# Kernel tuning notes

Hardware: AMD Instinct MI355X
Metric: run time of the kernel (lower is better)

The kernel has to match this reference:

```python
import jax, jax.numpy as jnp
import numpy as np

N_ENT = 100000
D = 128
N_EDGES = 1600000
B = 8192
EPS = 1e-5


def setup_inputs() -> dict:
    key = jax.random.key(0)
    ks = jax.random.split(key, 12)
    return {
        "E": jax.random.normal(ks[0], (N_ENT, D), jnp.float32),
        "gamma": jnp.ones((D,), jnp.float32),
        "beta": jnp.zeros((D,), jnp.float32),
        "W_gnn": jax.random.normal(ks[1], (D, D), jnp.float32) / np.sqrt(D),
        "b_gnn": jnp.zeros((D,), jnp.float32),
        "W_g": jax.random.normal(ks[2], (D,), jnp.float32) / np.sqrt(D),
        "b_g": jnp.zeros((), jnp.float32),
        "W_age": jax.random.normal(ks[3], (D, 7), jnp.float32) / np.sqrt(D),
        "b_age": jnp.zeros((7,), jnp.float32),
        "W_occ": jax.random.normal(ks[4], (D, 21), jnp.float32) / np.sqrt(D),
        "b_occ": jnp.zeros((21,), jnp.float32),
        "src": jax.random.randint(ks[5], (N_EDGES,), 0, N_ENT, jnp.int32),
        "dst": jax.random.randint(ks[6], (N_EDGES,), 0, N_ENT, jnp.int32),
        "neighbor": jax.random.randint(ks[7], (B,), 0, N_ENT, jnp.int32),
        "gender": jax.random.randint(ks[8], (B,), 0, 2, jnp.int32),
        "age": jax.random.randint(ks[9], (B,), 0, 7, jnp.int32),
        "occupation": jax.random.randint(ks[10], (B,), 0, 21, jnp.int32),
    }


def reference(E, gamma, beta, W_gnn, b_gnn, W_g, b_g, W_age, b_age, W_occ, b_occ,
              src, dst, neighbor, gender, age, occupation):
    n = E.shape[0]
    # encoder (embedding of all nodes) -> batchnorm over node axis
    mu = jnp.mean(E, axis=0)
    var = jnp.var(E, axis=0)
    h = (E - mu) * jax.lax.rsqrt(var + EPS) * gamma + beta  # [N, D]
    # gnn: mean neighbor aggregation over edge list, then linear + relu
    agg = jax.ops.segment_sum(h[src], dst, num_segments=n)  # [N, D]
    deg = jax.ops.segment_sum(jnp.ones_like(src, jnp.float32), dst, num_segments=n)
    agg = agg / jnp.maximum(deg, 1.0)[:, None]
    h = jax.nn.relu(agg @ W_gnn + b_gnn)  # [N, D]
    # gather walked-to nodes; gradient-reversal layer is identity in forward
    u = h[neighbor]  # [B, D]
    gender_pred = u @ W_g + b_g            # [B]
    age_pred = u @ W_age + b_age           # [B, 7]
    occ_pred = u @ W_occ + b_occ           # [B, 21]
    # mode == 'gender': BCEWithLogitsLoss (mean)
    z = gender.astype(jnp.float32)
    x = gender_pred
    loss_adv = jnp.mean(jnp.maximum(x, 0.0) - x * z + jnp.log1p(jnp.exp(-jnp.abs(x))))
    return (loss_adv, age_pred, gender_pred, occ_pred)
```

## Files before the change

### kernel.cpp

```cpp
#include <hip/hip_runtime.h>
#include <hip/hip_bf16.h>
#include <math.h>

#define N_ENT   100000
#define DIM     128
#define N_EDGES 1600000
#define BATCH   8192
#define EPS     1e-5f
#define CAP     64
#define NSTAT_BLK   512
#define NGATHER_BLK (BATCH / 4)

#define WS_SCALE     256
#define WS_SHIFT     384
#define WS_COUNT     512
#define WS_BCOUNT    528
#define WS_SLOTOF    8720
#define WS_BUCKET    108720
#define WS_SLOTHEAD  633008
#define WS_PARTIAL   895152
#define WS_HSUM      1026224

__global__ __launch_bounds__(256) void init_mark_kernel(const int* __restrict__ neighbor,
                                                        int* __restrict__ slot_of,
                                                        int* __restrict__ bcount,
                                                        int* __restrict__ count,
                                                        float* __restrict__ out_loss) {
    int n = blockIdx.x * 256 + threadIdx.x;
    if (n < BATCH) {
        bcount[n] = 0;
        slot_of[neighbor[n]] = -2;
    }
    if (n < 16) count[n] = 0;
    if (n == 0) out_loss[0] = 0.f;
}

__global__ __launch_bounds__(256) void compact_kernel(int* __restrict__ slot_of,
                                                      int* __restrict__ count) {
    int n = blockIdx.x * 256 + threadIdx.x;
    bool marked = (n < N_ENT && slot_of[n] == -2);
    unsigned long long m = __ballot(marked);
    int lane = threadIdx.x & 63;
    int wid = threadIdx.x >> 6;
    int prefix = __popcll(m & ((1ull << lane) - 1ull));
    __shared__ int wsum[4];
    __shared__ int base;
    if (lane == 0) wsum[wid] = __popcll(m);
    __syncthreads();
    if (threadIdx.x == 0) {
        base = atomicAdd(count, wsum[0] + wsum[1] + wsum[2] + wsum[3]);
    }
    __syncthreads();
    int wbase = 0;
    for (int i = 0; i < wid; ++i) wbase += wsum[i];
    if (marked) slot_of[n] = base + wbase + prefix;
}

__global__ __launch_bounds__(256) void edge_bucket_kernel(const int4* __restrict__ src4,
                                                          const int4* __restrict__ dst4,
                                                          const int* __restrict__ slot_of,
                                                          int* __restrict__ bcount,
                                                          int* __restrict__ bucket) {
    const int n4 = N_EDGES / 4;
    int tid = blockIdx.x * blockDim.x + threadIdx.x;
    int e0 = tid * 2;
    int e1 = tid * 2 + 1;
    if (e0 >= n4) return;
    int4 d0 = dst4[e0];
    int4 s0 = src4[e0];
    bool has1 = (e1 < n4);
    int4 d1 = has1 ? dst4[e1] : make_int4(0, 0, 0, 0);
    int4 s1 = has1 ? src4[e1] : make_int4(0, 0, 0, 0);
    int sl0 = slot_of[d0.x];
    int sl1 = slot_of[d0.y];
    int sl2 = slot_of[d0.z];
    int sl3 = slot_of[d0.w];
    int sl4 = has1 ? slot_of[d1.x] : -1;
    int sl5 = has1 ? slot_of[d1.y] : -1;
    int sl6 = has1 ? slot_of[d1.z] : -1;
    int sl7 = has1 ? slot_of[d1.w] : -1;
    if (sl0 >= 0) { int p = atomicAdd(&bcount[sl0], 1); if (p < CAP) bucket[sl0 * CAP + p] = s0.x; }
    if (sl1 >= 0) { int p = atomicAdd(&bcount[sl1], 1); if (p < CAP) bucket[sl1 * CAP + p] = s0.y; }
    if (sl2 >= 0) { int p = atomicAdd(&bcount[sl2], 1); if (p < CAP) bucket[sl2 * CAP + p] = s0.z; }
    if (sl3 >= 0) { int p = atomicAdd(&bcount[sl3], 1); if (p < CAP) bucket[sl3 * CAP + p] = s0.w; }
    if (sl4 >= 0) { int p = atomicAdd(&bcount[sl4], 1); if (p < CAP) bucket[sl4 * CAP + p] = s1.x; }
    if (sl5 >= 0) { int p = atomicAdd(&bcount[sl5], 1); if (p < CAP) bucket[sl5 * CAP + p] = s1.y; }
    if (sl6 >= 0) { int p = atomicAdd(&bcount[sl6], 1); if (p < CAP) bucket[sl6 * CAP + p] = s1.z; }
    if (sl7 >= 0) { int p = atomicAdd(&bcount[sl7], 1); if (p < CAP) bucket[sl7 * CAP + p] = s1.w; }
}

__global__ __launch_bounds__(256) void stats_gather_kernel(const float4* __restrict__ E4,
                                                           const int* __restrict__ count,
                                                           const int* __restrict__ bcount,
                                                           const int* __restrict__ bucket,
                                                           float* __restrict__ hsum,
                                                           float* __restrict__ partial) {
    int t = threadIdx.x;
    if (blockIdx.x < NGATHER_BLK) {
        int slot = blockIdx.x * 4 + (t >> 6);
        int U = count[0];
        if (slot >= U) return;
        int lane = t & 63;
        int q = lane & 31;
        int sub = lane >> 5;
        int dg = bcount[slot];
        int m = dg < CAP ? dg : CAP;
        const int* bk = bucket + slot * CAP;
        float ax = 0.f, ay = 0.f, az = 0.f, aw = 0.f;
        int i = sub;
        for (; i + 6 < m; i += 8) {
            int r0 = bk[i], r1 = bk[i + 2], r2 = bk[i + 4], r3 = bk[i + 6];
            float4 v0 = E4[(size_t)r0 * 32 + q];
            float4 v1 = E4[(size_t)r1 * 32 + q];
            float4 v2 = E4[(size_t)r2 * 32 + q];
            float4 v3 = E4[(size_t)r3 * 32 + q];
            ax += v0.x + v1.x + v2.x + v3.x;
            ay += v0.y + v1.y + v2.y + v3.y;
            az += v0.z + v1.z + v2.z + v3.z;
            aw += v0.w + v1.w + v2.w + v3.w;
        }
        for (; i < m; i += 2) {
            int r0 = bk[i];
            float4 v0 = E4[(size_t)r0 * 32 + q];
            ax += v0.x; ay += v0.y; az += v0.z; aw += v0.w;
        }
        ax += __shfl_down(ax, 32);
        ay += __shfl_down(ay, 32);
        az += __shfl_down(az, 32);
        aw += __shfl_down(aw, 32);
        if (sub == 0) {
            float4 o; o.x = ax; o.y = ay; o.z = az; o.w = aw;
            ((float4*)(hsum + (size_t)slot * DIM))[q] = o;
        }
        return;
    }
    int sid = blockIdx.x - NGATHER_BLK;
    int cg = t & 31;
    int rs = t >> 5;
    const int STRIDE = NSTAT_BLK * 8;
    float sx = 0.f, sy = 0.f, sz = 0.f, sw = 0.f;
    float qx = 0.f, qy = 0.f, qz = 0.f, qw = 0.f;
    const float4 z4 = make_float4(0.f, 0.f, 0.f, 0.f);
    for (int r = sid * 8 + rs; r < N_ENT; r += 4 * STRIDE) {
        int r1 = r + STRIDE, r2 = r + 2 * STRIDE, r3 = r + 3 * STRIDE;
        float4 v0 = E4[(size_t)r * 32 + cg];
        float4 v1 = (r1 < N_ENT) ? E4[(size_t)r1 * 32 + cg] : z4;
        float4 v2 = (r2 < N_ENT) ? E4[(size_t)r2 * 32 + cg] : z4;
        float4 v3 = (r3 < N_ENT) ? E4[(size_t)r3 * 32 + cg] : z4;
        sx += v0.x + v1.x + v2.x + v3.x;
        sy += v0.y + v1.y + v2.y + v3.y;
        sz += v0.z + v1.z + v2.z + v3.z;
        sw += v0.w + v1.w + v2.w + v3.w;
        qx += v0.x * v0.x + v1.x * v1.x + v2.x * v2.x + v3.x * v3.x;
        qy += v0.y * v0.y + v1.y * v1.y + v2.y * v2.y + v3.y * v3.y;
        qz += v0.z * v0.z + v1.z * v1.z + v2.z * v2.z + v3.z * v3.z;
        qw += v0.w * v0.w + v1.w * v1.w + v2.w * v2.w + v3.w * v3.w;
    }
    __shared__ float sh[8 * 256];
    sh[0 * 256 + t] = sx; sh[1 * 256 + t] = sy;
    sh[2 * 256 + t] = sz; sh[3 * 256 + t] = sw;
    sh[4 * 256 + t] = qx; sh[5 * 256 + t] = qy;
    sh[6 * 256 + t] = qz; sh[7 * 256 + t] = qw;
    __syncthreads();
    for (int o = 128; o >= 32; o >>= 1) {
        if (t < o) {
#pragma unroll
            for (int j = 0; j < 8; ++j) sh[j * 256 + t] += sh[j * 256 + t + o];
        }
        __syncthreads();
    }
    if (t < 32) {
#pragma unroll
        for (int j = 0; j < 8; ++j)
            partial[sid * 256 + j * 32 + t] = sh[j * 256 + t];
    }
}

__global__ __launch_bounds__(256) void finalize_kernel(const float* __restrict__ partial,
                                                       const float* __restrict__ gamma,
                                                       const float* __restrict__ beta,
                                                       float* __restrict__ scale,
                                                       float* __restrict__ shift) {
    int t = threadIdx.x;
    float s = 0.f;
    for (int b = 0; b < NSTAT_BLK; ++b) s += partial[b * 256 + t];
    __shared__ float tot[256];
    tot[t] = s;
    __syncthreads();
    if (t < 128) {
        int ti = t >> 2, j = t & 3;
        const float invn = 1.0f / (float)N_ENT;
        float mu = tot[j * 32 + ti] * invn;
        float var = tot[(j + 4) * 32 + ti] * invn - mu * mu;
        float rs = rsqrtf(var + EPS);
        float sc = gamma[t] * rs;
        scale[t] = sc;
        shift[t] = beta[t] - mu * sc;
    }
}

#define HW_LD 132

__global__ __launch_bounds__(256) void gemm_heads_kernel(const float* __restrict__ hsum,
                                                         const int* __restrict__ bcount,
                                                         const float* __restrict__ scale,
                                                         const float* __restrict__ shift,
                                                         const float4* __restrict__ W4,
                                                         const float4* __restrict__ bias4,
                                                         const float* __restrict__ W_g,
                                                         const float* __restrict__ b_g,
                                                         const float* __restrict__ W_age,
                                                         const float* __restrict__ b_age,
                                                         const float* __restrict__ W_occ,
                                                         const float* __restrict__ b_occ,
                                                         float* __restrict__ slot_heads) {
    __shared__ float A_s[32 * 128];
    __shared__ float HW[29 * HW_LD];
    __shared__ float hb[32];
    int t = threadIdx.x;
    int rowbase = blockIdx.x * 32;

    const float4* S4 = (const float4*)(hsum + (size_t)rowbase * DIM);
    const float4* sc4 = (const float4*)scale;
    const float4* sf4 = (const float4*)shift;
#pragma unroll
    for (int i = 0; i < 4; ++i) {
        int f4 = t + i * 256;
        int row = f4 >> 5;
        int cgl = f4 & 31;
        float fdg = (float)bcount[rowbase + row];
        float rd = 1.0f / fmaxf(fdg, 1.0f);
        float4 v = S4[f4];
        float4 sc = sc4[cgl];
        float4 sf = sf4[cgl];
        float4 o;
        o.x = (v.x * sc.x + fdg * sf.x) * rd;
        o.y = (v.y * sc.y + fdg * sf.y) * rd;
        o.z = (v.z * sc.z + fdg * sf.z) * rd;
        o.w = (v.w * sc.w + fdg * sf.w) * rd;
        ((float4*)A_s)[f4] = o;
    }
    for (int idx = t; idx < 29 * 128; idx += 256) {
        int h = idx >> 7;
        int d = idx & 127;
        float v;
        if (h < 7)       v = W_age[d * 7 + h];
        else if (h < 28) v = W_occ[d * 21 + (h - 7)];
        else             v = W_g[d];
        HW[h * HW_LD + d] = v;
    }
    if (t < 29) hb[t] = (t < 7) ? b_age[t] : (t < 28) ? b_occ[t - 7] : b_g[0];
    __syncthreads();

    int cg = t & 31;
    int rg = t >> 5;
    int r0 = rg * 4;
    float acc[4][4] = {{0.f}};
#pragma unroll 4
    for (int k = 0; k < 128; ++k) {
        float4 wv = W4[k * 32 + cg];
#pragma unroll
        for (int i = 0; i < 4; ++i) {
            float a = A_s[(r0 + i) * 128 + k];
            acc[i][0] += a * wv.x;
            acc[i][1] += a * wv.y;
            acc[i][2] += a * wv.z;
            acc[i][3] += a * wv.w;
        }
    }
    float4 bv = bias4[cg];
    __syncthreads();
#pragma unroll
    for (int i = 0; i < 4; ++i) {
        float4 o;
        o.x = fmaxf(acc[i][0] + bv.x, 0.f);
        o.y = fmaxf(acc[i][1] + bv.y, 0.f);
        o.z = fmaxf(acc[i][2] + bv.z, 0.f);
        o.w = fmaxf(acc[i][3] + bv.w, 0.f);
        ((float4*)A_s)[(r0 + i) * 32 + cg] = o;
    }
    __syncthreads();

#pragma unroll
    for (int i = 0; i < 4; ++i) {
        int task = t + i * 256;
        int row = task >> 5;
        int h = task & 31;
        if (h < 29) {
            const float4* h4 = (const float4*)(A_s + row * 128);
            const float4* w4 = (const float4*)(HW + h * HW_LD);
            float a0 = hb[h], a1 = 0.f, a2 = 0.f, a3 = 0.f;
#pragma unroll 8
            for (int dd = 0; dd < 32; ++dd) {
                float4 hv = h4[dd];
                float4 wv = w4[dd];
                a0 += hv.x * wv.x;
                a1 += hv.y * wv.y;
                a2 += hv.z * wv.z;
                a3 += hv.w * wv.w;
            }
            slot_heads[(size_t)(rowbase + row) * 32 + h] = a0 + a1 + a2 + a3;
        }
    }
}

__global__ __launch_bounds__(256) void map_loss_kernel(const float* __restrict__ slot_heads,
                                                       const int* __restrict__ slot_of,
                                                       const int* __restrict__ neighbor,
                                                       const int* __restrict__ gender,
                                                       float* __restrict__ out_age,
                                                       float* __restrict__ out_gender,
                                                       float* __restrict__ out_occ,
                                                       float* __restrict__ out_loss) {
    int b = blockIdx.x * 256 + threadIdx.x;
    float val = 0.f;
    if (b < BATCH) {
        int slot = slot_of[neighbor[b]];
        const float* hs = slot_heads + (size_t)slot * 32;
#pragma unroll
        for (int c = 0; c < 7; ++c)  out_age[b * 7 + c] = hs[c];
#pragma unroll
        for (int c = 0; c < 21; ++c) out_occ[b * 21 + c] = hs[7 + c];
        float x = hs[28];
        out_gender[b] = x;
        float z = (float)gender[b];
        val = fmaxf(x, 0.f) - x * z + log1pf(expf(-fabsf(x)));
    }
    __shared__ float sh[256];
    sh[threadIdx.x] = val;
    __syncthreads();
    for (int o = 128; o > 0; o >>= 1) {
        if (threadIdx.x < o) sh[threadIdx.x] += sh[threadIdx.x + o];
        __syncthreads();
    }
    if (threadIdx.x == 0) atomicAdd(out_loss, sh[0] * (1.0f / (float)BATCH));
}

extern "C" void kernel_launch(void* const* d_in, const int* in_sizes, int n_in,
                              void* d_out, int out_size, void* d_ws, size_t ws_size,
                              hipStream_t stream) {
    const float* E      = (const float*)d_in[0];
    const float* gamma  = (const float*)d_in[1];
    const float* beta   = (const float*)d_in[2];
    const float* W_gnn  = (const float*)d_in[3];
    const float* b_gnn  = (const float*)d_in[4];
    const float* W_g    = (const float*)d_in[5];
    const float* b_g    = (const float*)d_in[6];
    const float* W_age  = (const float*)d_in[7];
    const float* b_age  = (const float*)d_in[8];
    const float* W_occ  = (const float*)d_in[9];
    const float* b_occ  = (const float*)d_in[10];
    const int*   src    = (const int*)d_in[11];
    const int*   dst    = (const int*)d_in[12];
    const int*   neigh  = (const int*)d_in[13];
    const int*   gender = (const int*)d_in[14];

    float* ws      = (float*)d_ws;
    int*   wsi     = (int*)d_ws;
    float* scale   = ws + WS_SCALE;
    float* shift   = ws + WS_SHIFT;
    int*   count   = wsi + WS_COUNT;
    int*   bcount  = wsi + WS_BCOUNT;
    int*   slot_of = wsi + WS_SLOTOF;
    int*   bucket  = wsi + WS_BUCKET;
    float* slot_hd = ws + WS_SLOTHEAD;
    float* partial = ws + WS_PARTIAL;
    float* hsum    = ws + WS_HSUM;

    float* out       = (float*)d_out;
    float* out_loss  = out;
    float* out_age   = out + 1;
    float* out_gen   = out + 1 + BATCH * 7;
    float* out_occ   = out + 1 + BATCH * 7 + BATCH;

    init_mark_kernel<<<BATCH / 256, 256, 0, stream>>>(neigh, slot_of, bcount, count, out_loss);
    compact_kernel<<<(N_ENT + 255) / 256, 256, 0, stream>>>(slot_of, count);
    {
        const int n4 = N_EDGES / 4;
        int nthreads = (n4 + 1) / 2;
        edge_bucket_kernel<<<(nthreads + 255) / 256, 256, 0, stream>>>(
            (const int4*)src, (const int4*)dst, slot_of, bcount, bucket);
    }
    stats_gather_kernel<<<NGATHER_BLK + NSTAT_BLK, 256, 0, stream>>>(
        (const float4*)E, count, bcount, bucket, hsum, partial);
    finalize_kernel<<<1, 256, 0, stream>>>(partial, gamma, beta, scale, shift);
    gemm_heads_kernel<<<BATCH / 32, 256, 0, stream>>>(
        hsum, bcount, scale, shift,
        (const float4*)W_gnn, (const float4*)b_gnn,
        W_g, b_g, W_age, b_age, W_occ, b_occ, slot_hd);
    map_loss_kernel<<<BATCH / 256, 256, 0, stream>>>(slot_hd, slot_of, neigh, gender,
                                                     out_age, out_gen, out_occ, out_loss);
}
```

Baseline: 206.2 us.

## Drop slot compaction, fuse stats with init and finalize with edge bucketing

```diff
diff --git a/kernel.cpp b/kernel.cpp
--- a/kernel.cpp
+++ b/kernel.cpp
@@ -9,7 +9,6 @@
 #define EPS     1e-5f
 #define CAP     64
 #define NSTAT_BLK   512
-#define NGATHER_BLK (BATCH / 4)
 
 #define WS_SCALE     256
 #define WS_SHIFT     384
@@ -21,48 +20,95 @@
 #define WS_PARTIAL   895152
 #define WS_HSUM      1026224
 
-__global__ __launch_bounds__(256) void init_mark_kernel(const int* __restrict__ neighbor,
-                                                        int* __restrict__ slot_of,
-                                                        int* __restrict__ bcount,
-                                                        int* __restrict__ count,
-                                                        float* __restrict__ out_loss) {
-    int n = blockIdx.x * 256 + threadIdx.x;
-    if (n < BATCH) {
-        bcount[n] = 0;
-        slot_of[neighbor[n]] = -2;
-    }
-    if (n < 16) count[n] = 0;
-    if (n == 0) out_loss[0] = 0.f;
-}
-
-__global__ __launch_bounds__(256) void compact_kernel(int* __restrict__ slot_of,
-                                                      int* __restrict__ count) {
-    int n = blockIdx.x * 256 + threadIdx.x;
-    bool marked = (n < N_ENT && slot_of[n] == -2);
-    unsigned long long m = __ballot(marked);
-    int lane = threadIdx.x & 63;
-    int wid = threadIdx.x >> 6;
-    int prefix = __popcll(m & ((1ull << lane) - 1ull));
-    __shared__ int wsum[4];
-    __shared__ int base;
-    if (lane == 0) wsum[wid] = __popcll(m);
-    __syncthreads();
-    if (threadIdx.x == 0) {
-        base = atomicAdd(count, wsum[0] + wsum[1] + wsum[2] + wsum[3]);
-    }
-    __syncthreads();
-    int wbase = 0;
-    for (int i = 0; i < wid; ++i) wbase += wsum[i];
-    if (marked) slot_of[n] = base + wbase + prefix;
-}
-
-__global__ __launch_bounds__(256) void edge_bucket_kernel(const int4* __restrict__ src4,
-                                                          const int4* __restrict__ dst4,
-                                                          const int* __restrict__ slot_of,
-                                                          int* __restrict__ bcount,
-                                                          int* __restrict__ bucket) {
+__global__ __launch_bounds__(256) void stats_init_kernel(const float4* __restrict__ E4,
+                                                         const int* __restrict__ neighbor,
+                                                         int* __restrict__ slot_of,
+                                                         int* __restrict__ bcount,
+                                                         float* __restrict__ out_loss,
+                                                         float* __restrict__ partial) {
+    int t = threadIdx.x;
+    if (blockIdx.x >= NSTAT_BLK) {
+        int n = (blockIdx.x - NSTAT_BLK) * 256 + t;
+        if (n < BATCH) {
+            bcount[n] = 0;
+            slot_of[neighbor[n]] = n;
+        }
+        if (n == 0) out_loss[0] = 0.f;
+        return;
+    }
+    int sid = blockIdx.x;
+    int cg = t & 31;
+    int rs = t >> 5;
+    const int STRIDE = NSTAT_BLK * 8;
+    float sx = 0.f, sy = 0.f, sz = 0.f, sw = 0.f;
+    float qx = 0.f, qy = 0.f, qz = 0.f, qw = 0.f;
+    const float4 z4 = make_float4(0.f, 0.f, 0.f, 0.f);
+    for (int r = sid * 8 + rs; r < N_ENT; r += 8 * STRIDE) {
+        float4 v[8];
+#pragma unroll
+        for (int k = 0; k < 8; ++k) {
+            int rr = r + k * STRIDE;
+            v[k] = (rr < N_ENT) ? E4[(size_t)rr * 32 + cg] : z4;
+        }
+#pragma unroll
+        for (int k = 0; k < 8; ++k) {
+            sx += v[k].x; sy += v[k].y; sz += v[k].z; sw += v[k].w;
+            qx += v[k].x * v[k].x; qy += v[k].y * v[k].y;
+            qz += v[k].z * v[k].z; qw += v[k].w * v[k].w;
+        }
+    }
+    __shared__ float sh[8 * 256];
+    sh[0 * 256 + t] = sx; sh[1 * 256 + t] = sy;
+    sh[2 * 256 + t] = sz; sh[3 * 256 + t] = sw;
+    sh[4 * 256 + t] = qx; sh[5 * 256 + t] = qy;
+    sh[6 * 256 + t] = qz; sh[7 * 256 + t] = qw;
+    __syncthreads();
+    for (int o = 128; o >= 32; o >>= 1) {
+        if (t < o) {
+#pragma unroll
+            for (int j = 0; j < 8; ++j) sh[j * 256 + t] += sh[j * 256 + t + o];
+        }
+        __syncthreads();
+    }
+    if (t < 32) {
+#pragma unroll
+        for (int j = 0; j < 8; ++j)
+            partial[sid * 256 + j * 32 + t] = sh[j * 256 + t];
+    }
+}
+
+__global__ __launch_bounds__(256) void edge_finalize_kernel(const int4* __restrict__ src4,
+                                                            const int4* __restrict__ dst4,
+                                                            const int* __restrict__ slot_of,
+                                                            int* __restrict__ bcount,
+                                                            int* __restrict__ bucket,
+                                                            const float* __restrict__ partial,
+                                                            const float* __restrict__ gamma,
+                                                            const float* __restrict__ beta,
+                                                            float* __restrict__ scale,
+                                                            float* __restrict__ shift) {
+    if (blockIdx.x == 0) {
+        int t = threadIdx.x;
+        float s = 0.f;
+#pragma unroll 16
+        for (int b = 0; b < NSTAT_BLK; ++b) s += partial[b * 256 + t];
+        __shared__ float tot[256];
+        tot[t] = s;
+        __syncthreads();
+        if (t < 128) {
+            int ti = t >> 2, j = t & 3;
+            const float invn = 1.0f / (float)N_ENT;
+            float mu = tot[j * 32 + ti] * invn;
+            float var = tot[(j + 4) * 32 + ti] * invn - mu * mu;
+            float rs = rsqrtf(var + EPS);
+            float sc = gamma[t] * rs;
+            scale[t] = sc;
+            shift[t] = beta[t] - mu * sc;
+        }
+        return;
+    }
     const int n4 = N_EDGES / 4;
-    int tid = blockIdx.x * blockDim.x + threadIdx.x;
+    int tid = (blockIdx.x - 1) * blockDim.x + threadIdx.x;
     int e0 = tid * 2;
     int e1 = tid * 2 + 1;
     if (e0 >= n4) return;
@@ -89,113 +135,59 @@
     if (sl7 >= 0) { int p = atomicAdd(&bcount[sl7], 1); if (p < CAP) bucket[sl7 * CAP + p] = s1.w; }
 }
 
-__global__ __launch_bounds__(256) void stats_gather_kernel(const float4* __restrict__ E4,
-                                                           const int* __restrict__ count,
-                                                           const int* __restrict__ bcount,
-                                                           const int* __restrict__ bucket,
-                                                           float* __restrict__ hsum,
-                                                           float* __restrict__ partial) {
+__global__ __launch_bounds__(256) void gather_kernel(const float4* __restrict__ E4,
+                                                     const int* __restrict__ bcount,
+                                                     const int* __restrict__ bucket,
+                                                     float* __restrict__ hsum) {
     int t = threadIdx.x;
-    if (blockIdx.x < NGATHER_BLK) {
-        int slot = blockIdx.x * 4 + (t >> 6);
-        int U = count[0];
-        if (slot >= U) return;
-        int lane = t & 63;
-        int q = lane & 31;
-        int sub = lane >> 5;
-        int dg = bcount[slot];
-        int m = dg < CAP ? dg : CAP;
-        const int* bk = bucket + slot * CAP;
-        float ax = 0.f, ay = 0.f, az = 0.f, aw = 0.f;
-        int i = sub;
-        for (; i + 6 < m; i += 8) {
-            int r0 = bk[i], r1 = bk[i + 2], r2 = bk[i + 4], r3 = bk[i + 6];
-            float4 v0 = E4[(size_t)r0 * 32 + q];
-            float4 v1 = E4[(size_t)r1 * 32 + q];
-            float4 v2 = E4[(size_t)r2 * 32 + q];
-            float4 v3 = E4[(size_t)r3 * 32 + q];
-            ax += v0.x + v1.x + v2.x + v3.x;
-            ay += v0.y + v1.y + v2.y + v3.y;
-            az += v0.z + v1.z + v2.z + v3.z;
-            aw += v0.w + v1.w + v2.w + v3.w;
-        }
-        for (; i < m; i += 2) {
-            int r0 = bk[i];
-            float4 v0 = E4[(size_t)r0 * 32 + q];
-            ax += v0.x; ay += v0.y; az += v0.z; aw += v0.w;
-        }
-        ax += __shfl_down(ax, 32);
-        ay += __shfl_down(ay, 32);
-        az += __shfl_down(az, 32);
-        aw += __shfl_down(aw, 32);
-        if (sub == 0) {
-            float4 o; o.x = ax; o.y = ay; o.z = az; o.w = aw;
-            ((float4*)(hsum + (size_t)slot * DIM))[q] = o;
-        }
-        return;
-    }
-    int sid = blockIdx.x - NGATHER_BLK;
-    int cg = t & 31;
-    int rs = t >> 5;
-    const int STRIDE = NSTAT_BLK * 8;
-    float sx = 0.f, sy = 0.f, sz = 0.f, sw = 0.f;
-    float qx = 0.f, qy = 0.f, qz = 0.f, qw = 0.f;
-    const float4 z4 = make_float4(0.f, 0.f, 0.f, 0.f);
-    for (int r = sid * 8 + rs; r < N_ENT; r += 4 * STRIDE) {
-        int r1 = r + STRIDE, r2 = r + 2 * STRIDE, r3 = r + 3 * STRIDE;
-        float4 v0 = E4[(size_t)r * 32 + cg];
-        float4 v1 = (r1 < N_ENT) ? E4[(size_t)r1 * 32 + cg] : z4;
-        float4 v2 = (r2 < N_ENT) ? E4[(size_t)r2 * 32 + cg] : z4;
-        float4 v3 = (r3 < N_ENT) ? E4[(size_t)r3 * 32 + cg] : z4;
-        sx += v0.x + v1.x + v2.x + v3.x;
-        sy += v0.y + v1.y + v2.y + v3.y;
-        sz += v0.z + v1.z + v2.z + v3.z;
-        sw += v0.w + v1.w + v2.w + v3.w;
-        qx += v0.x * v0.x + v1.x * v1.x + v2.x * v2.x + v3.x * v3.x;
-        qy += v0.y * v0.y + v1.y * v1.y + v2.y * v2.y + v3.y * v3.y;
-        qz += v0.z * v0.z + v1.z * v1.z + v2.z * v2.z + v3.z * v3.z;
-        qw += v0.w * v0.w + v1.w * v1.w + v2.w * v2.w + v3.w * v3.w;
-    }
-    __shared__ float sh[8 * 256];
-    sh[0 * 256 + t] = sx; sh[1 * 256 + t] = sy;
-    sh[2 * 256 + t] = sz; sh[3 * 256 + t] = sw;
-    sh[4 * 256 + t] = qx; sh[5 * 256 + t] = qy;
-    sh[6 * 256 + t] = qz; sh[7 * 256 + t] = qw;
-    __syncthreads();
-    for (int o = 128; o >= 32; o >>= 1) {
-        if (t < o) {
-#pragma unroll
-            for (int j = 0; j < 8; ++j) sh[j * 256 + t] += sh[j * 256 + t + o];
-        }
-        __syncthreads();
-    }
-    if (t < 32) {
-#pragma unroll
-        for (int j = 0; j < 8; ++j)
-            partial[sid * 256 + j * 32 + t] = sh[j * 256 + t];
-    }
-}
-
-__global__ __launch_bounds__(256) void finalize_kernel(const float* __restrict__ partial,
-                                                       const float* __restrict__ gamma,
-                                                       const float* __restrict__ beta,
-                                                       float* __restrict__ scale,
-                                                       float* __restrict__ shift) {
-    int t = threadIdx.x;
-    float s = 0.f;
-    for (int b = 0; b < NSTAT_BLK; ++b) s += partial[b * 256 + t];
-    __shared__ float tot[256];
-    tot[t] = s;
-    __syncthreads();
-    if (t < 128) {
-        int ti = t >> 2, j = t & 3;
-        const float invn = 1.0f / (float)N_ENT;
-        float mu = tot[j * 32 + ti] * invn;
-        float var = tot[(j + 4) * 32 + ti] * invn - mu * mu;
-        float rs = rsqrtf(var + EPS);
-        float sc = gamma[t] * rs;
-        scale[t] = sc;
-        shift[t] = beta[t] - mu * sc;
+    int slot = blockIdx.x * 4 + (t >> 6);
+    int lane = t & 63;
+    int q = lane & 31;
+    int sub = lane >> 5;
+    int dg = bcount[slot];
+    int m = dg < CAP ? dg : CAP;
+    const int* bk = bucket + slot * CAP;
+    float ax = 0.f, ay = 0.f, az = 0.f, aw = 0.f;
+    int i = sub;
+    for (; i + 14 < m; i += 16) {
+        int r0 = bk[i], r1 = bk[i + 2], r2 = bk[i + 4], r3 = bk[i + 6];
+        int r4 = bk[i + 8], r5 = bk[i + 10], r6 = bk[i + 12], r7 = bk[i + 14];
+        float4 v0 = E4[(size_t)r0 * 32 + q];
+        float4 v1 = E4[(size_t)r1 * 32 + q];
+        float4 v2 = E4[(size_t)r2 * 32 + q];
+        float4 v3 = E4[(size_t)r3 * 32 + q];
+        float4 v4 = E4[(size_t)r4 * 32 + q];
+        float4 v5 = E4[(size_t)r5 * 32 + q];
+        float4 v6 = E4[(size_t)r6 * 32 + q];
+        float4 v7 = E4[(size_t)r7 * 32 + q];
+        ax += v0.x + v1.x + v2.x + v3.x + v4.x + v5.x + v6.x + v7.x;
+        ay += v0.y + v1.y + v2.y + v3.y + v4.y + v5.y + v6.y + v7.y;
+        az += v0.z + v1.z + v2.z + v3.z + v4.z + v5.z + v6.z + v7.z;
+        aw += v0.w + v1.w + v2.w + v3.w + v4.w + v5.w + v6.w + v7.w;
+    }
+    for (; i + 6 < m; i += 8) {
+        int r0 = bk[i], r1 = bk[i + 2], r2 = bk[i + 4], r3 = bk[i + 6];
+        float4 v0 = E4[(size_t)r0 * 32 + q];
+        float4 v1 = E4[(size_t)r1 * 32 + q];
+        float4 v2 = E4[(size_t)r2 * 32 + q];
+        float4 v3 = E4[(size_t)r3 * 32 + q];
+        ax += v0.x + v1.x + v2.x + v3.x;
+        ay += v0.y + v1.y + v2.y + v3.y;
+        az += v0.z + v1.z + v2.z + v3.z;
+        aw += v0.w + v1.w + v2.w + v3.w;
+    }
+    for (; i < m; i += 2) {
+        int r0 = bk[i];
+        float4 v0 = E4[(size_t)r0 * 32 + q];
+        ax += v0.x; ay += v0.y; az += v0.z; aw += v0.w;
+    }
+    ax += __shfl_down(ax, 32);
+    ay += __shfl_down(ay, 32);
+    az += __shfl_down(az, 32);
+    aw += __shfl_down(aw, 32);
+    if (sub == 0) {
+        float4 o; o.x = ax; o.y = ay; o.z = az; o.w = aw;
+        ((float4*)(hsum + (size_t)slot * DIM))[q] = o;
     }
 }
 
@@ -359,7 +351,6 @@
     int*   wsi     = (int*)d_ws;
     float* scale   = ws + WS_SCALE;
     float* shift   = ws + WS_SHIFT;
-    int*   count   = wsi + WS_COUNT;
     int*   bcount  = wsi + WS_BCOUNT;
     int*   slot_of = wsi + WS_SLOTOF;
     int*   bucket  = wsi + WS_BUCKET;
@@ -373,17 +364,18 @@
     float* out_gen   = out + 1 + BATCH * 7;
     float* out_occ   = out + 1 + BATCH * 7 + BATCH;
 
-    init_mark_kernel<<<BATCH / 256, 256, 0, stream>>>(neigh, slot_of, bcount, count, out_loss);
-    compact_kernel<<<(N_ENT + 255) / 256, 256, 0, stream>>>(slot_of, count);
+    stats_init_kernel<<<NSTAT_BLK + BATCH / 256, 256, 0, stream>>>(
+        (const float4*)E, neigh, slot_of, bcount, out_loss, partial);
     {
         const int n4 = N_EDGES / 4;
         int nthreads = (n4 + 1) / 2;
-        edge_bucket_kernel<<<(nthreads + 255) / 256, 256, 0, stream>>>(
-            (const int4*)src, (const int4*)dst, slot_of, bcount, bucket);
-    }
-    stats_gather_kernel<<<NGATHER_BLK + NSTAT_BLK, 256, 0, stream>>>(
-        (const float4*)E, count, bcount, bucket, hsum, partial);
-    finalize_kernel<<<1, 256, 0, stream>>>(partial, gamma, beta, scale, shift);
+        int eblocks = (nthreads + 255) / 256;
+        edge_finalize_kernel<<<1 + eblocks, 256, 0, stream>>>(
+            (const int4*)src, (const int4*)dst, slot_of, bcount, bucket,
+            partial, gamma, beta, scale, shift);
+    }
+    gather_kernel<<<BATCH / 4, 256, 0, stream>>>(
+        (const float4*)E, bcount, bucket, hsum);
     gemm_heads_kernel<<<BATCH / 32, 256, 0, stream>>>(
         hsum, bcount, scale, shift,
         (const float4*)W_gnn, (const float4*)b_gnn,
```

Result: faster. 186.5 us (-9.5%).
